# Performance work log

Measured on AMD Instinct MI355X. Metric: run time of the kernel, lower is better.

Reference implementation:

```python
import jax, jax.numpy as jnp
import numpy as np

N = 20000
E = 640000
C_IN = 256
C_OUT = 256
K = 2
EPS = 1e-12


def setup_inputs() -> dict:
    key = jax.random.key(0)
    k1, k2, k3, k4, k5 = jax.random.split(key, 5)
    x = jax.random.normal(k1, (N, C_IN), dtype=jnp.float32)
    edge_index = jax.random.randint(k2, (2, E), 0, N, dtype=jnp.int64)
    edge_weights = jax.random.uniform(k3, (E,), dtype=jnp.float32)
    lin_w = jax.random.normal(k4, (C_OUT, C_IN), dtype=jnp.float32) / np.sqrt(C_IN)
    lin_b = jax.random.normal(k5, (C_OUT,), dtype=jnp.float32) * 0.01
    return {"x": x, "edge_index": edge_index, "edge_weights": edge_weights,
            "lin_w": lin_w, "lin_b": lin_b}


def reference(x, edge_index, edge_weights, lin_w, lin_b):
    row, col = edge_index[0], edge_index[1]  # source -> target

    # F.normalize(x, p=2, dim=-1)
    nrm = jnp.sqrt(jnp.sum(x * x, axis=-1, keepdims=True))
    x = x / jnp.maximum(nrm, EPS)

    # gcn_norm with add_self_loops=False (PyG): deg over target nodes
    deg = jax.ops.segment_sum(edge_weights, col, num_segments=N)
    deg_inv_sqrt = jnp.where(deg > 0, 1.0 / jnp.sqrt(deg), 0.0)
    norm = deg_inv_sqrt[row] * edge_weights * deg_inv_sqrt[col]  # [E]

    # K-hop propagation: out[col] += norm * x[row]
    for _ in range(K):
        msgs = norm[:, None] * x[row]                     # [E, C]
        x = jax.ops.segment_sum(msgs, col, num_segments=N)

    # Linear layer of SGConv
    return x @ lin_w.T + lin_b
```

## Files before the change

### kernel.cpp

```cpp
#include <hip/hip_runtime.h>
#include <hip/hip_bf16.h>

#define N_NODES 20000
#define N_EDGES 640000
#define C 256
#define S 96
#define CNTS 16

#define SCATTER_BLOCKS 2500
#define WCONV_BLOCKS 256
#define NORM_BLOCKS 10000

#define BPAD 264

typedef __attribute__((ext_vector_type(8))) short short8;
typedef __attribute__((ext_vector_type(4))) float float4v;
typedef __attribute__((ext_vector_type(4))) unsigned uint4v;

__device__ inline unsigned short f2bf(float f) {
    unsigned u = __float_as_uint(f);
    unsigned r = (u + 0x7fffu + ((u >> 16) & 1u)) >> 16;
    return (unsigned short)r;
}
__device__ inline float bf_lo(unsigned u) { return __uint_as_float(u << 16); }
__device__ inline float bf_hi(unsigned u) { return __uint_as_float(u & 0xffff0000u); }
__device__ inline float bf_hi_raw(unsigned u) { return __uint_as_float(u); }

__global__ __launch_bounds__(256) void scatter_kernel(
        const int* __restrict__ ei, const float* __restrict__ w,
        const float* __restrict__ lw,
        int* __restrict__ cnt, unsigned* __restrict__ csr,
        unsigned short* __restrict__ Wb) {
    int b = blockIdx.x;
    int t = threadIdx.x;
    if (b < SCATTER_BLOCKS) {
        __shared__ int okw[4];
        unsigned long long m = __ballot(ei[2 * t + 1] == 0);
        if ((t & 63) == 0) okw[t >> 6] = (m == 0xFFFFFFFFFFFFFFFFull) ? 1 : 0;
        __syncthreads();
        int flag = okw[0] & okw[1] & okw[2] & okw[3];
        int e = b * 256 + t;
        int r, c;
        if (flag) { r = ei[2 * e]; c = ei[2 * (N_EDGES + e)]; }
        else      { r = ei[e];     c = ei[N_EDGES + e]; }
        float wf = w[e];
        int pos = atomicAdd(&cnt[c * CNTS], 1);
        atomicAdd((float*)&cnt[c * CNTS + 1], wf);
        if (pos < S) csr[c * S + pos] = (unsigned)r | ((unsigned)f2bf(wf) << 16);
    } else {
        int idx = (b - SCATTER_BLOCKS) * 256 + t;
        Wb[idx] = f2bf(lw[idx]);
    }
}

__global__ __launch_bounds__(256) void norm_kernel(
        const float* __restrict__ x, const int* __restrict__ cnt,
        float* __restrict__ dis, unsigned char* __restrict__ ncap,
        unsigned* __restrict__ xs32) {
    int t = threadIdx.x;
    int half = t >> 7;
    int tt = t & 127;
    int i = blockIdx.x * 2 + half;
    float2 v = ((const float2*)x)[(size_t)i * 128 + tt];
    float ss = v.x * v.x + v.y * v.y;
    #pragma unroll
    for (int o = 32; o > 0; o >>= 1) ss += __shfl_down(ss, o, 64);
    __shared__ float wsum[4];
    if ((t & 63) == 0) wsum[t >> 6] = ss;
    __syncthreads();
    float tot = wsum[half * 2] + wsum[half * 2 + 1];
    float deg = ((const float*)cnt)[i * CNTS + 1];
    float d = (deg > 0.0f) ? rsqrtf(deg) : 0.0f;
    float inv = d / fmaxf(sqrtf(tot), 1e-12f);
    xs32[(size_t)i * 128 + tt] =
        (unsigned)f2bf(v.x * inv) | ((unsigned)f2bf(v.y * inv) << 16);
    if (tt == 0) {
        dis[i] = d;
        int n = cnt[i * CNTS];
        ncap[i] = (unsigned char)(n > S ? S : n);
    }
}

#define MAC4(ee, vv)                                              \
    {   float wf = __uint_as_float(ee.y);                         \
        c0.x += wf * bf_lo(vv.x); c0.y += wf * bf_hi_raw(vv.x);   \
        c1.x += wf * bf_lo(vv.y); c1.y += wf * bf_hi_raw(vv.y);   \
        c2.x += wf * bf_lo(vv.z); c2.y += wf * bf_hi_raw(vv.z);   \
        c3.x += wf * bf_lo(vv.w); c3.y += wf * bf_hi_raw(vv.w); }

template <int POW>
__global__ __launch_bounds__(256) void gather_kernel(const unsigned char* __restrict__ ncap,
                                                     const unsigned* __restrict__ csr,
                                                     const float* __restrict__ dis,
                                                     const unsigned* __restrict__ in,
                                                     unsigned* __restrict__ out) {
    __shared__ uint2 st_all[4][S];
    int wvi = threadIdx.x >> 6;
    int lane = threadIdx.x & 63;
    int i = blockIdx.x * 4 + wvi;
    float d = dis[i];
    int n = ncap[i];
    int nup = (n + 7) & ~7;
    uint2* st = st_all[wvi];
    if (lane < n) {
        unsigned p = __builtin_nontemporal_load(&csr[i * S + lane]);
        st[lane] = make_uint2((p & 0xffffu) << 9, p & 0xffff0000u);
    }
    if (lane + 64 < n) {
        unsigned p = __builtin_nontemporal_load(&csr[i * S + lane + 64]);
        st[lane + 64] = make_uint2((p & 0xffffu) << 9, p & 0xffff0000u);
    }
    {
        int k = n + lane;
        if (k < nup) st[k] = make_uint2(0u, 0u);
    }
    __builtin_amdgcn_wave_barrier();

    int grp = lane >> 5;
    unsigned hb = (unsigned)(lane & 31) << 4;
    const char* base = (const char*)in;
    float2 c0 = {0.f, 0.f}, c1 = {0.f, 0.f}, c2 = {0.f, 0.f}, c3 = {0.f, 0.f};
    int j = 0;
    for (; j + 16 <= nup; j += 16) {
        uint2 e0 = st[j + grp];
        uint2 e1 = st[j + 2 + grp];
        uint2 e2 = st[j + 4 + grp];
        uint2 e3 = st[j + 6 + grp];
        uint2 e4 = st[j + 8 + grp];
        uint2 e5 = st[j + 10 + grp];
        uint2 e6 = st[j + 12 + grp];
        uint2 e7 = st[j + 14 + grp];
        uint4v v0 = *(const uint4v*)(base + (e0.x + hb));
        uint4v v1 = *(const uint4v*)(base + (e1.x + hb));
        uint4v v2 = *(const uint4v*)(base + (e2.x + hb));
        uint4v v3 = *(const uint4v*)(base + (e3.x + hb));
        uint4v v4 = *(const uint4v*)(base + (e4.x + hb));
        uint4v v5 = *(const uint4v*)(base + (e5.x + hb));
        uint4v v6 = *(const uint4v*)(base + (e6.x + hb));
        uint4v v7 = *(const uint4v*)(base + (e7.x + hb));
        MAC4(e0, v0) MAC4(e1, v1) MAC4(e2, v2) MAC4(e3, v3)
        MAC4(e4, v4) MAC4(e5, v5) MAC4(e6, v6) MAC4(e7, v7)
    }
    if (j < nup) {
        uint2 e0 = st[j + grp];
        uint2 e1 = st[j + 2 + grp];
        uint2 e2 = st[j + 4 + grp];
        uint2 e3 = st[j + 6 + grp];
        uint4v v0 = *(const uint4v*)(base + (e0.x + hb));
        uint4v v1 = *(const uint4v*)(base + (e1.x + hb));
        uint4v v2 = *(const uint4v*)(base + (e2.x + hb));
        uint4v v3 = *(const uint4v*)(base + (e3.x + hb));
        MAC4(e0, v0) MAC4(e1, v1) MAC4(e2, v2) MAC4(e3, v3)
    }
    c0.x += __shfl_down(c0.x, 32, 64); c0.y += __shfl_down(c0.y, 32, 64);
    c1.x += __shfl_down(c1.x, 32, 64); c1.y += __shfl_down(c1.y, 32, 64);
    c2.x += __shfl_down(c2.x, 32, 64); c2.y += __shfl_down(c2.y, 32, 64);
    c3.x += __shfl_down(c3.x, 32, 64); c3.y += __shfl_down(c3.y, 32, 64);
    if (lane < 32) {
        float sc = (POW == 2) ? d * d : d;
        uint4v r;
        r.x = (unsigned)f2bf(c0.x * sc) | ((unsigned)f2bf(c0.y * sc) << 16);
        r.y = (unsigned)f2bf(c1.x * sc) | ((unsigned)f2bf(c1.y * sc) << 16);
        r.z = (unsigned)f2bf(c2.x * sc) | ((unsigned)f2bf(c2.y * sc) << 16);
        r.w = (unsigned)f2bf(c3.x * sc) | ((unsigned)f2bf(c3.y * sc) << 16);
        __builtin_nontemporal_store(r, (uint4v*)(out + (size_t)i * 128) + lane);
    }
}

__global__ __launch_bounds__(256, 4) void gemm_kernel(const unsigned short* __restrict__ h,
                                                      const unsigned short* __restrict__ Wb,
                                                      const float* __restrict__ b,
                                                      float* __restrict__ out) {
    __shared__ unsigned short Bs[64 * BPAD];
    int t = threadIdx.x;
    int wv = t >> 6;
    int lane = t & 63;
    int m = lane & 15;
    int q = lane >> 4;
    int rg = blockIdx.x >> 2;
    int cg = blockIdx.x & 3;
    #pragma unroll
    for (int it = 0; it < 8; it++) {
        int ch = it * 256 + t;
        int col = ch >> 5;
        int off8 = (ch & 31) * 8;
        *(uint4v*)(Bs + col * BPAD + off8) =
            *(const uint4v*)(Wb + (size_t)(cg * 64 + col) * C + off8);
    }
    __syncthreads();

    int rowbase = rg * 64 + wv * 16;
    int rowA = rowbase + m;
    if (rowA > N_NODES - 1) rowA = N_NODES - 1;
    float4v acc[4];
    #pragma unroll
    for (int nt = 0; nt < 4; nt++) acc[nt] = (float4v){0.f, 0.f, 0.f, 0.f};
    #pragma unroll
    for (int kt = 0; kt < 8; kt++) {
        int kb = kt * 32 + q * 8;
        short8 a = *(const short8*)(h + (size_t)rowA * C + kb);
        #pragma unroll
        for (int nt = 0; nt < 4; nt++) {
            short8 bb = *(const short8*)(Bs + (nt * 16 + m) * BPAD + kb);
            acc[nt] = __builtin_amdgcn_mfma_f32_16x16x32_bf16(a, bb, acc[nt], 0, 0, 0);
        }
    }
    #pragma unroll
    for (int nt = 0; nt < 4; nt++) {
        int col = cg * 64 + nt * 16 + m;
        float bias = b[col];
        #pragma unroll
        for (int r = 0; r < 4; r++) {
            int ro = rowbase + q * 4 + r;
            if (ro < N_NODES)
                __builtin_nontemporal_store(acc[nt][r] + bias, &out[(size_t)ro * C + col]);
        }
    }
}

extern "C" void kernel_launch(void* const* d_in, const int* in_sizes, int n_in,
                              void* d_out, int out_size, void* d_ws, size_t ws_size,
                              hipStream_t stream) {
    const float* x  = (const float*)d_in[0];
    const int*   ei = (const int*)d_in[1];
    const float* w  = (const float*)d_in[2];
    const float* lw = (const float*)d_in[3];
    const float* lb = (const float*)d_in[4];
    float* out = (float*)d_out;

    char* ws = (char*)d_ws;
    size_t off = 0;
    auto alloc = [&](size_t bytes) -> void* {
        void* p = ws + off;
        off = (off + bytes + 255) & ~(size_t)255;
        return p;
    };
    unsigned* bufA   = (unsigned*)alloc((size_t)N_NODES * 128 * 4);
    unsigned* bufB   = (unsigned*)alloc((size_t)N_NODES * 128 * 4);
    float* dis       = (float*)alloc((size_t)N_NODES * 4);
    int*   cnt       = (int*)alloc((size_t)N_NODES * CNTS * 4);
    unsigned* csr    = (unsigned*)alloc((size_t)N_NODES * S * 4);
    unsigned short* Wb = (unsigned short*)alloc((size_t)C * C * 2);
    unsigned char* ncap = (unsigned char*)alloc((size_t)N_NODES);
    (void)ws_size; (void)in_sizes; (void)n_in; (void)out_size;

    (void)hipMemsetAsync(cnt, 0, (size_t)N_NODES * CNTS * 4, stream);

    scatter_kernel<<<SCATTER_BLOCKS + WCONV_BLOCKS, 256, 0, stream>>>(
        ei, w, lw, cnt, csr, Wb);
    norm_kernel<<<NORM_BLOCKS, 256, 0, stream>>>(x, cnt, dis, ncap, bufA);
    gather_kernel<2><<<N_NODES / 4, 256, 0, stream>>>(ncap, csr, dis, bufA, bufB);
    gather_kernel<1><<<N_NODES / 4, 256, 0, stream>>>(ncap, csr, dis, bufB, bufA);
    gemm_kernel<<<313 * 4, 256, 0, stream>>>(
        (const unsigned short*)bufA, Wb, lb, out);
}
```

Measured before the change: 232.5 us.

## Fuse normalize into scatter launch and derive degree from CSR weights

The L2 row normalization moves into the same launch as edge scattering and weight conversion, so it no longer waits for degrees to be complete. The float atomic degree accumulation is dropped. A small per-node kernel instead sums the bf16 edge weights stored in the CSR to produce deg^-1/2 and the capped neighbor count. The first gather pass folds the source-side deg^-1/2 into each edge weight by indexing dis[src], since x is no longer pre-scaled. This gives up one atomic per edge and one dependency, but adds a kernel launch and extra CSR and dis reads. The degree is now summed from bf16-rounded weights and only over the first S edges, which may change precision.

```diff
diff --git a/kernel.cpp b/kernel.cpp
--- a/kernel.cpp
+++ b/kernel.cpp
@@ -8,8 +8,8 @@
 #define CNTS 16
 
 #define SCATTER_BLOCKS 2500
+#define NORM_BLOCKS 10000
 #define WCONV_BLOCKS 256
-#define NORM_BLOCKS 10000
 
 #define BPAD 264
 
@@ -26,11 +26,11 @@
 __device__ inline float bf_hi(unsigned u) { return __uint_as_float(u & 0xffff0000u); }
 __device__ inline float bf_hi_raw(unsigned u) { return __uint_as_float(u); }
 
-__global__ __launch_bounds__(256) void scatter_kernel(
+__global__ __launch_bounds__(256) void fused_pre_kernel(
         const int* __restrict__ ei, const float* __restrict__ w,
-        const float* __restrict__ lw,
+        const float* __restrict__ x, const float* __restrict__ lw,
         int* __restrict__ cnt, unsigned* __restrict__ csr,
-        unsigned short* __restrict__ Wb) {
+        unsigned* __restrict__ xs32, unsigned short* __restrict__ Wb) {
     int b = blockIdx.x;
     int t = threadIdx.x;
     if (b < SCATTER_BLOCKS) {
@@ -43,41 +43,44 @@
         int r, c;
         if (flag) { r = ei[2 * e]; c = ei[2 * (N_EDGES + e)]; }
         else      { r = ei[e];     c = ei[N_EDGES + e]; }
-        float wf = w[e];
         int pos = atomicAdd(&cnt[c * CNTS], 1);
-        atomicAdd((float*)&cnt[c * CNTS + 1], wf);
-        if (pos < S) csr[c * S + pos] = (unsigned)r | ((unsigned)f2bf(wf) << 16);
+        if (pos < S) csr[c * S + pos] = (unsigned)r | ((unsigned)f2bf(w[e]) << 16);
+    } else if (b < SCATTER_BLOCKS + NORM_BLOCKS) {
+        int half = t >> 7;
+        int tt = t & 127;
+        int i = (b - SCATTER_BLOCKS) * 2 + half;
+        float2 v = ((const float2*)x)[(size_t)i * 128 + tt];
+        float ss = v.x * v.x + v.y * v.y;
+        #pragma unroll
+        for (int o = 32; o > 0; o >>= 1) ss += __shfl_down(ss, o, 64);
+        __shared__ float wsum[4];
+        if ((t & 63) == 0) wsum[t >> 6] = ss;
+        __syncthreads();
+        float tot = wsum[half * 2] + wsum[half * 2 + 1];
+        float inv = 1.0f / fmaxf(sqrtf(tot), 1e-12f);
+        xs32[(size_t)i * 128 + tt] =
+            (unsigned)f2bf(v.x * inv) | ((unsigned)f2bf(v.y * inv) << 16);
     } else {
-        int idx = (b - SCATTER_BLOCKS) * 256 + t;
+        int idx = (b - SCATTER_BLOCKS - NORM_BLOCKS) * 256 + t;
         Wb[idx] = f2bf(lw[idx]);
     }
 }
 
-__global__ __launch_bounds__(256) void norm_kernel(
-        const float* __restrict__ x, const int* __restrict__ cnt,
-        float* __restrict__ dis, unsigned char* __restrict__ ncap,
-        unsigned* __restrict__ xs32) {
-    int t = threadIdx.x;
-    int half = t >> 7;
-    int tt = t & 127;
-    int i = blockIdx.x * 2 + half;
-    float2 v = ((const float2*)x)[(size_t)i * 128 + tt];
-    float ss = v.x * v.x + v.y * v.y;
-    #pragma unroll
-    for (int o = 32; o > 0; o >>= 1) ss += __shfl_down(ss, o, 64);
-    __shared__ float wsum[4];
-    if ((t & 63) == 0) wsum[t >> 6] = ss;
-    __syncthreads();
-    float tot = wsum[half * 2] + wsum[half * 2 + 1];
-    float deg = ((const float*)cnt)[i * CNTS + 1];
-    float d = (deg > 0.0f) ? rsqrtf(deg) : 0.0f;
-    float inv = d / fmaxf(sqrtf(tot), 1e-12f);
-    xs32[(size_t)i * 128 + tt] =
-        (unsigned)f2bf(v.x * inv) | ((unsigned)f2bf(v.y * inv) << 16);
-    if (tt == 0) {
-        dis[i] = d;
-        int n = cnt[i * CNTS];
-        ncap[i] = (unsigned char)(n > S ? S : n);
+__global__ void deg_dis_kernel(const unsigned* __restrict__ csr, const int* __restrict__ cnt,
+                               float* __restrict__ dis, unsigned char* __restrict__ ncap) {
+    int wv = threadIdx.x >> 6;
+    int lane = threadIdx.x & 63;
+    int i = blockIdx.x * 4 + wv;
+    int n = cnt[i * CNTS];
+    if (n > S) n = S;
+    float s = 0.0f;
+    if (lane < n) s = bf_hi(__builtin_nontemporal_load(&csr[i * S + lane]));
+    if (lane + 64 < n) s += bf_hi(__builtin_nontemporal_load(&csr[i * S + lane + 64]));
+    #pragma unroll
+    for (int o = 32; o > 0; o >>= 1) s += __shfl_down(s, o, 64);
+    if (lane == 0) {
+        dis[i] = (s > 0.0f) ? rsqrtf(s) : 0.0f;
+        ncap[i] = (unsigned char)n;
     }
 }
 
@@ -88,7 +91,7 @@
         c2.x += wf * bf_lo(vv.z); c2.y += wf * bf_hi_raw(vv.z);   \
         c3.x += wf * bf_lo(vv.w); c3.y += wf * bf_hi_raw(vv.w); }
 
-template <int POW>
+template <int POW, int SRC_DIS>
 __global__ __launch_bounds__(256) void gather_kernel(const unsigned char* __restrict__ ncap,
                                                      const unsigned* __restrict__ csr,
                                                      const float* __restrict__ dis,
@@ -104,11 +107,17 @@
     uint2* st = st_all[wvi];
     if (lane < n) {
         unsigned p = __builtin_nontemporal_load(&csr[i * S + lane]);
-        st[lane] = make_uint2((p & 0xffffu) << 9, p & 0xffff0000u);
+        unsigned s = p & 0xffffu;
+        float wv = bf_hi(p);
+        if (SRC_DIS) wv *= dis[s];
+        st[lane] = make_uint2(s << 9, __float_as_uint(wv));
     }
     if (lane + 64 < n) {
         unsigned p = __builtin_nontemporal_load(&csr[i * S + lane + 64]);
-        st[lane + 64] = make_uint2((p & 0xffffu) << 9, p & 0xffff0000u);
+        unsigned s = p & 0xffffu;
+        float wv = bf_hi(p);
+        if (SRC_DIS) wv *= dis[s];
+        st[lane + 64] = make_uint2(s << 9, __float_as_uint(wv));
     }
     {
         int k = n + lane;
@@ -246,11 +255,11 @@
 
     (void)hipMemsetAsync(cnt, 0, (size_t)N_NODES * CNTS * 4, stream);
 
-    scatter_kernel<<<SCATTER_BLOCKS + WCONV_BLOCKS, 256, 0, stream>>>(
-        ei, w, lw, cnt, csr, Wb);
-    norm_kernel<<<NORM_BLOCKS, 256, 0, stream>>>(x, cnt, dis, ncap, bufA);
-    gather_kernel<2><<<N_NODES / 4, 256, 0, stream>>>(ncap, csr, dis, bufA, bufB);
-    gather_kernel<1><<<N_NODES / 4, 256, 0, stream>>>(ncap, csr, dis, bufB, bufA);
+    fused_pre_kernel<<<SCATTER_BLOCKS + NORM_BLOCKS + WCONV_BLOCKS, 256, 0, stream>>>(
+        ei, w, x, lw, cnt, csr, bufA, Wb);
+    deg_dis_kernel<<<N_NODES / 4, 256, 0, stream>>>(csr, cnt, dis, ncap);
+    gather_kernel<2, 1><<<N_NODES / 4, 256, 0, stream>>>(ncap, csr, dis, bufA, bufB);
+    gather_kernel<1, 0><<<N_NODES / 4, 256, 0, stream>>>(ncap, csr, dis, bufB, bufA);
     gemm_kernel<<<313 * 4, 256, 0, stream>>>(
         (const unsigned short*)bufA, Wb, lb, out);
 }
```

Result: faster. 198.5 us (-14.6%).
